# Performance work log

Hardware: AMD Instinct MI355X
Metric: run time of the kernel (lower is better)

## Reference

```python
import jax, jax.numpy as jnp
import numpy as np

N_CLASSES = 91

def setup_inputs() -> dict:
    key = jax.random.key(0)
    k1, k2 = jax.random.split(key)
    B, H, W = 32, 1024, 1024
    inputs = jax.random.randint(k1, (B, H, W), 0, N_CLASSES, dtype=jnp.int32)
    targets = jax.random.randint(k2, (B, H, W), 0, N_CLASSES, dtype=jnp.int32)
    smooth = jnp.ones((1,), dtype=jnp.float32)  # original default smooth=1
    return {"inputs": inputs, "targets": targets, "smooth": smooth}

def reference(inputs, targets, smooth):
    # Single-pass histogram formulation of the original 91-iteration loop.
    B = inputs.shape[0]
    x = inputs.reshape(B, -1)   # [B, N] int labels
    t = targets.reshape(B, -1)  # [B, N]
    rows = jnp.arange(B)[:, None]
    # per-class counts: cnt_x[b,c] = #pixels with x==c (== a.sum per class)
    cnt_x = jnp.zeros((B, N_CLASSES), jnp.float32).at[rows, x].add(1.0)
    cnt_t = jnp.zeros((B, N_CLASSES), jnp.float32).at[rows, t].add(1.0)
    # intersection[b,c] = #pixels with x==t==c; route mismatches to a dump bin
    match = jnp.where(x == t, x, N_CLASSES)
    inter = jnp.zeros((B, N_CLASSES + 1), jnp.float32).at[rows, match].add(1.0)[:, :N_CLASSES]
    union = cnt_x + cnt_t - inter  # total - intersection
    s = smooth[0]
    iou = (inter + s) / (union + s)  # [B, C]
    return iou.mean(axis=1)          # sum_IoU / n_classes, shape [B]
```

## Files before the change

kernel.cpp:

```cpp
#include <hip/hip_runtime.h>

#define NC 91
#define NBIN 182
#define NB 32
#define HW (1024 * 1024)
#define NT 256
#define PPT 64
#define PIX_PER_BLOCK (NT * PPT)
#define STRIDE 260

__global__ __launch_bounds__(256) void hist_kernel(const int* __restrict__ x,
                                                   const int* __restrict__ t,
                                                   int* __restrict__ g_hist) {
    __shared__ unsigned char s_h[NBIN * STRIDE];

    const int tid = threadIdx.x;

    {
        unsigned int* p = (unsigned int*)s_h;
        for (int i = tid; i < NBIN * STRIDE / 4; i += NT) p[i] = 0u;
    }
    __syncthreads();

    unsigned char* h = s_h + tid;

    const int b = blockIdx.y;
    const long base = (long)b * HW + (long)blockIdx.x * PIX_PER_BLOCK;
    const int4* __restrict__ x4 = (const int4*)(x + base);
    const int4* __restrict__ t4 = (const int4*)(t + base);

#pragma unroll 4
    for (int i = 0; i < PPT / 4; ++i) {
        int4 xv = x4[i * NT + tid];
        int4 tv = t4[i * NT + tid];
        int u0 = xv.x, u1 = xv.y, u2 = xv.z, u3 = xv.w;
        int v0 = (xv.x == tv.x) ? (NC + xv.x) : tv.x;
        int v1 = (xv.y == tv.y) ? (NC + xv.y) : tv.y;
        int v2 = (xv.z == tv.z) ? (NC + xv.z) : tv.z;
        int v3 = (xv.w == tv.w) ? (NC + xv.w) : tv.w;
        h[u0 * STRIDE] += 1;
        h[v0 * STRIDE] += 1;
        h[u1 * STRIDE] += 1;
        h[v1 * STRIDE] += 1;
        h[u2 * STRIDE] += 1;
        h[v2 * STRIDE] += 1;
        h[u3 * STRIDE] += 1;
        h[v3 * STRIDE] += 1;
    }
    __syncthreads();

    for (int c = tid; c < NBIN; c += NT) {
        const unsigned int* row = (const unsigned int*)(s_h + c * STRIDE);
        unsigned int s = 0;
#pragma unroll
        for (int k = 0; k < 64; ++k) {
            unsigned int d = row[k];
#if __has_builtin(__builtin_amdgcn_udot4)
            s = __builtin_amdgcn_udot4(d, 0x01010101u, s, false);
#else
            s += (d & 0xffu) + ((d >> 8) & 0xffu) + ((d >> 16) & 0xffu) + (d >> 24);
#endif
        }
        atomicAdd(&g_hist[b * NBIN + c], (int)s);
    }
}

__global__ __launch_bounds__(64) void finalize_kernel(const int* __restrict__ g_hist,
                                                      const float* __restrict__ smooth,
                                                      float* __restrict__ out) {
    const int b = blockIdx.x;
    const int lane = threadIdx.x;
    const float s = smooth[0];
    float acc = 0.0f;
    for (int c = lane; c < NC; c += 64) {
        float un = (float)g_hist[b * NBIN + c];
        float in = (float)g_hist[b * NBIN + NC + c];
        acc += (in + s) / (un + s);
    }
#pragma unroll
    for (int off = 32; off > 0; off >>= 1)
        acc += __shfl_down(acc, off, 64);
    if (lane == 0) out[b] = acc / (float)NC;
}

extern "C" void kernel_launch(void* const* d_in, const int* in_sizes, int n_in,
                              void* d_out, int out_size, void* d_ws, size_t ws_size,
                              hipStream_t stream) {
    const int* x = (const int*)d_in[0];
    const int* t = (const int*)d_in[1];
    const float* smooth = (const float*)d_in[2];
    float* out = (float*)d_out;

    int* g_hist = (int*)d_ws;

    hipMemsetAsync(d_ws, 0, NB * NBIN * sizeof(int), stream);

    dim3 grid(HW / PIX_PER_BLOCK, NB);
    hist_kernel<<<grid, NT, 0, stream>>>(x, t, g_hist);
    finalize_kernel<<<NB, 64, 0, stream>>>(g_hist, smooth, out);
}
```

Baseline: 281.2 us.

## Pack four byte counters per LDS word with per-thread word-wise histogram updates

The per-thread shared-memory histogram changes from byte-addressed rows (stride 260) to 32-bit words that each hold four 8-bit bins, laid out so each thread owns one column per word-row. Each pixel now does a word read-modify-write instead of a byte RMW, and when the two bins of a pixel land in the same word the update is merged. The final reduction is split across four threads per row using packed 16-bit partial sums, then combined. The aim is cheaper, bank-conflict-free LDS updates and a faster reduction, at the cost of extra shift and mask ALU work per pixel.

```diff
diff --git a/kernel.cpp b/kernel.cpp
--- a/kernel.cpp
+++ b/kernel.cpp
@@ -2,65 +2,79 @@
 
 #define NC 91
 #define NBIN 182
+#define NROWS 46
 #define NB 32
 #define HW (1024 * 1024)
 #define NT 256
 #define PPT 64
 #define PIX_PER_BLOCK (NT * PPT)
-#define STRIDE 260
+
 
 __global__ __launch_bounds__(256) void hist_kernel(const int* __restrict__ x,
                                                    const int* __restrict__ t,
                                                    int* __restrict__ g_hist) {
-    __shared__ unsigned char s_h[NBIN * STRIDE];
+    __shared__ unsigned int s_h[NROWS * 256];
+    __shared__ unsigned int s_part[NROWS][4][2];
 
     const int tid = threadIdx.x;
 
-    {
-        unsigned int* p = (unsigned int*)s_h;
-        for (int i = tid; i < NBIN * STRIDE / 4; i += NT) p[i] = 0u;
+    for (int i = tid; i < NROWS * 256; i += NT) s_h[i] = 0u;
+    __syncthreads();
+
+    const int b = blockIdx.y;
+    const long base = (long)b * HW + (long)blockIdx.x * PIX_PER_BLOCK;
+    const int4* __restrict__ x4 = (const int4*)(x + base) + tid;
+    const int4* __restrict__ t4 = (const int4*)(t + base) + tid;
+
+#pragma unroll 4
+    for (int i = 0; i < PPT / 4; ++i) {
+        int4 xv = x4[i * NT];
+        int4 tv = t4[i * NT];
+#define PIX(X, T) { \
+            int u = (X); \
+            int v = ((X) == (T)) ? (NC + (X)) : (T); \
+            int au = ((u >> 2) << 8) + tid; \
+            int av = ((v >> 2) << 8) + tid; \
+            unsigned mu = 1u << ((u & 3) << 3); \
+            unsigned mv = 1u << ((v & 3) << 3); \
+            unsigned ru = s_h[au]; \
+            unsigned rv = s_h[av]; \
+            bool same = (au == av); \
+            unsigned wu = ru + mu + (same ? mv : 0u); \
+            unsigned wv = same ? wu : (rv + mv); \
+            s_h[au] = wu; \
+            s_h[av] = wv; \
+        }
+        PIX(xv.x, tv.x)
+        PIX(xv.y, tv.y)
+        PIX(xv.z, tv.z)
+        PIX(xv.w, tv.w)
+#undef PIX
     }
     __syncthreads();
 
-    unsigned char* h = s_h + tid;
-
-    const int b = blockIdx.y;
-    const long base = (long)b * HW + (long)blockIdx.x * PIX_PER_BLOCK;
-    const int4* __restrict__ x4 = (const int4*)(x + base);
-    const int4* __restrict__ t4 = (const int4*)(t + base);
-
-#pragma unroll 4
-    for (int i = 0; i < PPT / 4; ++i) {
-        int4 xv = x4[i * NT + tid];
-        int4 tv = t4[i * NT + tid];
-        int u0 = xv.x, u1 = xv.y, u2 = xv.z, u3 = xv.w;
-        int v0 = (xv.x == tv.x) ? (NC + xv.x) : tv.x;
-        int v1 = (xv.y == tv.y) ? (NC + xv.y) : tv.y;
-        int v2 = (xv.z == tv.z) ? (NC + xv.z) : tv.z;
-        int v3 = (xv.w == tv.w) ? (NC + xv.w) : tv.w;
-        h[u0 * STRIDE] += 1;
-        h[v0 * STRIDE] += 1;
-        h[u1 * STRIDE] += 1;
-        h[v1 * STRIDE] += 1;
-        h[u2 * STRIDE] += 1;
-        h[v2 * STRIDE] += 1;
-        h[u3 * STRIDE] += 1;
-        h[v3 * STRIDE] += 1;
+    if (tid < NROWS * 4) {
+        const int row = tid >> 2, q = tid & 3;
+        const unsigned int* rp = s_h + row * 256 + q * 64;
+        unsigned slo = 0, shi = 0;
+#pragma unroll 8
+        for (int k = 0; k < 64; ++k) {
+            unsigned d = rp[(k + tid) & 63];
+            slo += d & 0x00FF00FFu;
+            shi += (d >> 8) & 0x00FF00FFu;
+        }
+        s_part[row][q][0] = slo;
+        s_part[row][q][1] = shi;
     }
     __syncthreads();
 
     for (int c = tid; c < NBIN; c += NT) {
-        const unsigned int* row = (const unsigned int*)(s_h + c * STRIDE);
-        unsigned int s = 0;
+        const int row = c >> 2, k = c & 3;
+        const int sel = k & 1, half = k >> 1;
+        unsigned s = 0;
 #pragma unroll
-        for (int k = 0; k < 64; ++k) {
-            unsigned int d = row[k];
-#if __has_builtin(__builtin_amdgcn_udot4)
-            s = __builtin_amdgcn_udot4(d, 0x01010101u, s, false);
-#else
-            s += (d & 0xffu) + ((d >> 8) & 0xffu) + ((d >> 16) & 0xffu) + (d >> 24);
-#endif
-        }
+        for (int q = 0; q < 4; ++q)
+            s += (s_part[row][q][sel] >> (16 * half)) & 0xFFFFu;
         atomicAdd(&g_hist[b * NBIN + c], (int)s);
     }
 }
```

Result: no change. 285.7 us (+1.6%).

## Replace per-thread byte histograms with shared joint confusion-matrix atomics

Applied to the files above, without the earlier changes.

Swaps the per-thread private uint8 histograms (182 bins x 256 threads) for a single 96x96 joint histogram of (input, target) pairs in shared memory, updated with LDS atomics. Union and intersection are then taken from row sums, column sums and the diagonal. Pixels per thread double, halving the block count and the number of global atomics per pixel. The cost is contended LDS atomics, one per pixel instead of two non-atomic byte increments, plus a heavier per-block reduction over the 96x96 matrix.

```diff
diff --git a/kernel.cpp b/kernel.cpp
--- a/kernel.cpp
+++ b/kernel.cpp
@@ -5,63 +5,67 @@
 #define NB 32
 #define HW (1024 * 1024)
 #define NT 256
-#define PPT 64
+#define PPT 128
 #define PIX_PER_BLOCK (NT * PPT)
-#define STRIDE 260
+#define JS 96
 
 __global__ __launch_bounds__(256) void hist_kernel(const int* __restrict__ x,
                                                    const int* __restrict__ t,
                                                    int* __restrict__ g_hist) {
-    __shared__ unsigned char s_h[NBIN * STRIDE];
+    __shared__ unsigned int J[JS * JS];
+    __shared__ unsigned int colpart[4][JS];
+    __shared__ unsigned int rowsum[JS], colsum[JS];
 
     const int tid = threadIdx.x;
+    for (int i = tid; i < JS * JS; i += NT) J[i] = 0u;
+    __syncthreads();
 
-    {
-        unsigned int* p = (unsigned int*)s_h;
-        for (int i = tid; i < NBIN * STRIDE / 4; i += NT) p[i] = 0u;
+    const int b = blockIdx.y;
+    const long base = (long)b * HW + (long)blockIdx.x * PIX_PER_BLOCK;
+    const int4* __restrict__ x4 = (const int4*)(x + base) + tid;
+    const int4* __restrict__ t4 = (const int4*)(t + base) + tid;
+
+#pragma unroll 4
+    for (int i = 0; i < PPT / 4; ++i) {
+        int4 xv = x4[i * NT];
+        int4 tv = t4[i * NT];
+        atomicAdd(&J[xv.x * JS + tv.x], 1u);
+        atomicAdd(&J[xv.y * JS + tv.y], 1u);
+        atomicAdd(&J[xv.z * JS + tv.z], 1u);
+        atomicAdd(&J[xv.w * JS + tv.w], 1u);
     }
     __syncthreads();
 
-    unsigned char* h = s_h + tid;
+    const int wave = tid >> 6, lane = tid & 63;
 
-    const int b = blockIdx.y;
-    const long base = (long)b * HW + (long)blockIdx.x * PIX_PER_BLOCK;
-    const int4* __restrict__ x4 = (const int4*)(x + base);
-    const int4* __restrict__ t4 = (const int4*)(t + base);
+    {
+        unsigned ca = 0, cb = 0;
+        const int m0 = wave * (JS / 4), m1 = m0 + (JS / 4);
+        for (int m = m0; m < m1; ++m) {
+            ca += J[m * JS + lane];
+            if (lane < JS - 64) cb += J[m * JS + 64 + lane];
+        }
+        colpart[wave][lane] = ca;
+        if (lane < JS - 64) colpart[wave][64 + lane] = cb;
+    }
 
-#pragma unroll 4
-    for (int i = 0; i < PPT / 4; ++i) {
-        int4 xv = x4[i * NT + tid];
-        int4 tv = t4[i * NT + tid];
-        int u0 = xv.x, u1 = xv.y, u2 = xv.z, u3 = xv.w;
-        int v0 = (xv.x == tv.x) ? (NC + xv.x) : tv.x;
-        int v1 = (xv.y == tv.y) ? (NC + xv.y) : tv.y;
-        int v2 = (xv.z == tv.z) ? (NC + xv.z) : tv.z;
-        int v3 = (xv.w == tv.w) ? (NC + xv.w) : tv.w;
-        h[u0 * STRIDE] += 1;
-        h[v0 * STRIDE] += 1;
-        h[u1 * STRIDE] += 1;
-        h[v1 * STRIDE] += 1;
-        h[u2 * STRIDE] += 1;
-        h[v2 * STRIDE] += 1;
-        h[u3 * STRIDE] += 1;
-        h[v3 * STRIDE] += 1;
+    for (int m = wave; m < JS; m += 4) {
+        unsigned r = J[m * JS + lane] + ((lane < JS - 64) ? J[m * JS + 64 + lane] : 0u);
+#pragma unroll
+        for (int off = 32; off > 0; off >>= 1) r += __shfl_down(r, off, 64);
+        if (lane == 0) rowsum[m] = r;
     }
     __syncthreads();
 
-    for (int c = tid; c < NBIN; c += NT) {
-        const unsigned int* row = (const unsigned int*)(s_h + c * STRIDE);
-        unsigned int s = 0;
-#pragma unroll
-        for (int k = 0; k < 64; ++k) {
-            unsigned int d = row[k];
-#if __has_builtin(__builtin_amdgcn_udot4)
-            s = __builtin_amdgcn_udot4(d, 0x01010101u, s, false);
-#else
-            s += (d & 0xffu) + ((d >> 8) & 0xffu) + ((d >> 16) & 0xffu) + (d >> 24);
-#endif
-        }
-        atomicAdd(&g_hist[b * NBIN + c], (int)s);
+    if (tid < JS)
+        colsum[tid] = colpart[0][tid] + colpart[1][tid] + colpart[2][tid] + colpart[3][tid];
+    __syncthreads();
+
+    if (tid < NC) {
+        unsigned diag = J[tid * JS + tid];
+        unsigned un = rowsum[tid] + colsum[tid] - diag;
+        atomicAdd(&g_hist[b * NBIN + tid], (int)un);
+        atomicAdd(&g_hist[b * NBIN + NC + tid], (int)diag);
     }
 }
 
```

After: 290.8 us. 1.03x slower.
